# Performance work log

Hardware: AMD Instinct MI355X
Metric: run time of the kernel (lower is better)

## Reference

```python
import jax, jax.numpy as jnp
import numpy as np

B, T, H = 4096, 64, 64        # sequences, time_step, n_hidden
OBS, ACT = 128, 32
EPS = 1e-12                    # tf.contrib layer_norm epsilon


def layer_norm(x, g, b):
    m = x.mean(-1, keepdims=True)
    v = x.var(-1, keepdims=True)
    return (x - m) * jax.lax.rsqrt(v + EPS) * g + b


def lstm_scan(xs, W, b):
    # xs: [T, B, D_in]; BasicLSTMCell with forget_bias=1.0
    h0 = jnp.zeros((xs.shape[1], H), xs.dtype)
    c0 = h0
    def step(carry, x_t):
        h, c = carry
        z = jnp.concatenate([x_t, h], axis=-1) @ W + b   # [B, 4H]
        i, j, f, o = jnp.split(z, 4, axis=-1)
        c = c * jax.nn.sigmoid(f + 1.0) + jax.nn.sigmoid(i) * jnp.tanh(j)
        h = jnp.tanh(c) * jax.nn.sigmoid(o)
        return (h, c), h
    _, hs = jax.lax.scan(step, (h0, c0), xs)
    return hs  # [T, B, H]


def setup_inputs() -> dict:
    key = jax.random.key(0)
    ks = jax.random.split(key, 10)
    u = lambda k, shp, s: jax.random.uniform(k, shp, jnp.float32, -s, s)
    return dict(
        obs=jax.random.normal(ks[0], (B * T, OBS), jnp.float32),
        action=jax.random.normal(ks[1], (B * T, ACT), jnp.float32),
        W1=u(ks[2], (OBS, 64), 0.1), b1=jnp.zeros(64), g1=jnp.ones(64), be1=jnp.zeros(64),
        W2=u(ks[3], (64 + ACT, 64), 0.1), b2=jnp.zeros(64), g2=jnp.ones(64), be2=jnp.zeros(64),
        Wf=u(ks[4], (64 + H, 4 * H), 0.08), bf=jnp.zeros(4 * H),
        Wb=u(ks[5], (64 + H, 4 * H), 0.08), bb=jnp.zeros(4 * H),
        wx=u(ks[6], (H,), 0.003), bx=jnp.zeros(()),
        wp=u(ks[7], (H,), 0.003), bp=jnp.zeros(()),
        gp=jnp.ones(T), bep=jnp.zeros(T),
        W3=u(ks[8], (T, T), 0.003), b3=jnp.zeros(T),
    )


def reference(obs, action, W1, b1, g1, be1, W2, b2, g2, be2,
              Wf, bf, Wb, bb, wx, bx, wp, bp, gp, bep, W3, b3):
    # MLP trunk
    x = jax.nn.relu(layer_norm(obs @ W1 + b1, g1, be1))
    x = jnp.concatenate([x, action], axis=-1)
    x = jax.nn.relu(layer_norm(x @ W2 + b2, g2, be2))
    # [B*T, 64] -> [T, B, 64] for scan
    x = x.reshape(B, T, 64).transpose(1, 0, 2)
    h_fw = lstm_scan(x, Wf, bf)                 # [T, B, H]
    h_bw = lstm_scan(x[::-1], Wb, bb)[::-1]     # [T, B, H]
    # tf.reshape of the (fw, bw) tuple stacks -> [2, B, T, H] -> [2B, T*H, 1]
    h = jnp.concatenate([h_fw.transpose(1, 0, 2), h_bw.transpose(1, 0, 2)], axis=0)  # [2B, T, H]
    # conv1d(kernel=H, stride=H) over flattened T*H axis == per-timestep dot
    xs = jnp.einsum('btd,d->bt', h, wx) + bx    # [2B, T] values
    ps = jnp.einsum('btd,d->bt', h, wp) + bp    # [2B, T] attention logits
    p = jax.nn.relu(layer_norm(ps, gp, bep))
    p = jax.nn.softmax(p @ W3 + b3, axis=-1)
    return jnp.sum(p * xs, axis=1)              # [2B]
```

## Files before the change

kernel.cpp:

```cpp
#include <hip/hip_runtime.h>
#include <hip/hip_bf16.h>

typedef __attribute__((ext_vector_type(8))) short s16x8;
typedef __attribute__((ext_vector_type(4))) float f32x4;
typedef __attribute__((ext_vector_type(4))) unsigned int u32x4;

#define MFMA(a,b,c) __builtin_amdgcn_mfma_f32_16x16x32_bf16((a),(b),(c),0,0,0)

__device__ __forceinline__ unsigned short bf16_rne(float f){
  unsigned int u = __float_as_uint(f);
  return (unsigned short)((u + 0x7FFFu + ((u >> 16) & 1u)) >> 16);
}
__device__ __forceinline__ float bf16_f32(unsigned short h){
  return __uint_as_float(((unsigned int)h) << 16);
}
__device__ __forceinline__ void split_hl(float f, short& hi, short& lo){
  unsigned short h = bf16_rne(f);
  float rem = f - bf16_f32(h);
  hi = (short)h;
  lo = (short)bf16_rne(rem);
}

__device__ __forceinline__ unsigned int cvt_pk_bf16(float a, float b){
  unsigned int r;
  asm("v_cvt_pk_bf16_f32 %0, %1, %2" : "=v"(r) : "v"(a), "v"(b));
  return r;
}

__device__ __forceinline__ void build_frag(const float* p, s16x8& fh, s16x8& fl){
  float4 v0 = *(const float4*)p;
  float4 v1 = *(const float4*)(p + 4);
  float vv[8] = {v0.x, v0.y, v0.z, v0.w, v1.x, v1.y, v1.z, v1.w};
  u32x4 th, tl;
  #pragma unroll
  for(int q = 0; q < 4; ++q){
    unsigned int h2 = cvt_pk_bf16(vv[2*q], vv[2*q+1]);
    float r0 = vv[2*q]     - __uint_as_float(h2 << 16);
    float r1 = vv[2*q + 1] - __uint_as_float(h2 & 0xffff0000u);
    th[q] = h2;
    tl[q] = cvt_pk_bf16(r0, r1);
  }
  fh = __builtin_bit_cast(s16x8, th);
  fl = __builtin_bit_cast(s16x8, tl);
}

__device__ __forceinline__ float sigm(float x){
  return __builtin_amdgcn_rcpf(1.0f + __expf(-x));
}
__device__ __forceinline__ float tanh_fast(float x){
  return 1.0f - 2.0f * __builtin_amdgcn_rcpf(__expf(2.0f * x) + 1.0f);
}

__global__ __launch_bounds__(256) void pack_kernel(
    const float* __restrict__ W1, const float* __restrict__ W2,
    const float* __restrict__ Wf, const float* __restrict__ Wb,
    unsigned short* __restrict__ w1p, unsigned short* __restrict__ w2p,
    unsigned short* __restrict__ wfp, unsigned short* __restrict__ wbp)
{
  int id = blockIdx.x * 256 + threadIdx.x;
  if(id < 8192){
    int t = id;
    int j = t & 7, lane = (t >> 3) & 63, nt = (t >> 9) & 3, kk = t >> 11;
    int k = kk * 32 + 8 * (lane >> 4) + j;
    int col = nt * 16 + (lane & 15);
    short h, l; split_hl(W1[k * 64 + col], h, l);
    w1p[t] = (unsigned short)h; w1p[8192 + t] = (unsigned short)l;
  } else if(id < 14336){
    int t = id - 8192;
    int j = t & 7, lane = (t >> 3) & 63, nt = (t >> 9) & 3, kk = t >> 11;
    int k = kk * 32 + 8 * (lane >> 4) + j;
    int col = nt * 16 + (lane & 15);
    short h, l; split_hl(W2[k * 64 + col], h, l);
    w2p[t] = (unsigned short)h; w2p[6144 + t] = (unsigned short)l;
  } else if(id < 47104){
    int t = id - 14336;
    int j = t & 7, lane = (t >> 3) & 63, dj = (t >> 9) & 3, kk = (t >> 11) & 3, gi = t >> 13;
    int k = kk * 32 + 8 * (lane >> 4) + j;
    int col = gi * 64 + dj * 16 + (lane & 15);
    short h, l; split_hl(Wf[k * 256 + col], h, l);
    wfp[t] = (unsigned short)h; wfp[32768 + t] = (unsigned short)l;
  } else if(id < 79872){
    int t = id - 47104;
    int j = t & 7, lane = (t >> 3) & 63, dj = (t >> 9) & 3, kk = (t >> 11) & 3, gi = t >> 13;
    int k = kk * 32 + 8 * (lane >> 4) + j;
    int col = gi * 64 + dj * 16 + (lane & 15);
    short h, l; split_hl(Wb[k * 256 + col], h, l);
    wbp[t] = (unsigned short)h; wbp[32768 + t] = (unsigned short)l;
  }
}

__global__ __launch_bounds__(256) void trunk_kernel(
    const float* __restrict__ obs, const float* __restrict__ actg,
    const float* __restrict__ b1, const float* __restrict__ g1, const float* __restrict__ be1,
    const float* __restrict__ b2, const float* __restrict__ g2, const float* __restrict__ be2,
    const unsigned short* __restrict__ w1p, const unsigned short* __restrict__ w2p,
    unsigned short* __restrict__ x2h, unsigned short* __restrict__ x2l)
{
  __shared__ __align__(16) float x1_t[64][68];

  const int tid = threadIdx.x;
  const int r0 = blockIdx.x * 64;
  const int w = tid >> 6, lane = tid & 63;
  const int l15 = lane & 15, l4 = lane >> 4;

  float b1v[4], g1v[4], be1v[4], b2v[4], g2v[4], be2v[4];
  #pragma unroll
  for(int nt = 0; nt < 4; ++nt){
    int col = nt * 16 + l15;
    b1v[nt] = b1[col]; g1v[nt] = g1[col]; be1v[nt] = be1[col];
    b2v[nt] = b2[col]; g2v[nt] = g2[col]; be2v[nt] = be2[col];
  }

  f32x4 acc1[4] = {{0,0,0,0},{0,0,0,0},{0,0,0,0},{0,0,0,0}};
  #pragma unroll
  for(int kk = 0; kk < 4; ++kk){
    s16x8 ah, al;
    build_frag(&obs[(size_t)(r0 + w * 16 + l15) * 128 + 8 * l4 + 32 * kk], ah, al);
    #pragma unroll
    for(int nt = 0; nt < 4; ++nt){
      s16x8 bh = *(const s16x8*)&w1p[(kk * 2048 + nt * 512) + lane * 8];
      s16x8 bl = *(const s16x8*)&w1p[8192 + (kk * 2048 + nt * 512) + lane * 8];
      acc1[nt] = MFMA(ah, bh, acc1[nt]);
      acc1[nt] = MFMA(ah, bl, acc1[nt]);
      acc1[nt] = MFMA(al, bh, acc1[nt]);
    }
  }

  #pragma unroll
  for(int r = 0; r < 4; ++r){
    float v[4];
    #pragma unroll
    for(int nt = 0; nt < 4; ++nt) v[nt] = acc1[nt][r] + b1v[nt];
    float s = (v[0] + v[1]) + (v[2] + v[3]);
    #pragma unroll
    for(int mm = 1; mm < 16; mm <<= 1) s += __shfl_xor(s, mm);
    float mean = s * (1.0f / 64.0f);
    float d[4]; float q = 0.f;
    #pragma unroll
    for(int nt = 0; nt < 4; ++nt){ d[nt] = v[nt] - mean; q += d[nt] * d[nt]; }
    #pragma unroll
    for(int mm = 1; mm < 16; mm <<= 1) q += __shfl_xor(q, mm);
    float rstd = rsqrtf(q * (1.0f / 64.0f) + 1e-12f);
    int row = w * 16 + l4 * 4 + r;
    #pragma unroll
    for(int nt = 0; nt < 4; ++nt)
      x1_t[row][nt * 16 + l15] = fmaxf(0.f, d[nt] * rstd * g1v[nt] + be1v[nt]);
  }
  __syncthreads();

  f32x4 acc2[4] = {{0,0,0,0},{0,0,0,0},{0,0,0,0},{0,0,0,0}};
  #pragma unroll
  for(int kk = 0; kk < 3; ++kk){
    s16x8 ah, al;
    if(kk < 2) build_frag(&x1_t[w * 16 + l15][8 * l4 + 32 * kk], ah, al);
    else       build_frag(&actg[(size_t)(r0 + w * 16 + l15) * 32 + 8 * l4], ah, al);
    #pragma unroll
    for(int nt = 0; nt < 4; ++nt){
      s16x8 bh = *(const s16x8*)&w2p[(kk * 2048 + nt * 512) + lane * 8];
      s16x8 bl = *(const s16x8*)&w2p[6144 + (kk * 2048 + nt * 512) + lane * 8];
      acc2[nt] = MFMA(ah, bh, acc2[nt]);
      acc2[nt] = MFMA(ah, bl, acc2[nt]);
      acc2[nt] = MFMA(al, bh, acc2[nt]);
    }
  }

  #pragma unroll
  for(int r = 0; r < 4; ++r){
    float v[4];
    #pragma unroll
    for(int nt = 0; nt < 4; ++nt) v[nt] = acc2[nt][r] + b2v[nt];
    float s = (v[0] + v[1]) + (v[2] + v[3]);
    #pragma unroll
    for(int mm = 1; mm < 16; mm <<= 1) s += __shfl_xor(s, mm);
    float mean = s * (1.0f / 64.0f);
    float d[4]; float q = 0.f;
    #pragma unroll
    for(int nt = 0; nt < 4; ++nt){ d[nt] = v[nt] - mean; q += d[nt] * d[nt]; }
    #pragma unroll
    for(int mm = 1; mm < 16; mm <<= 1) q += __shfl_xor(q, mm);
    float rstd = rsqrtf(q * (1.0f / 64.0f) + 1e-12f);
    size_t rowg = (size_t)(r0 + w * 16 + l4 * 4 + r);
    float xv[4];
    #pragma unroll
    for(int nt = 0; nt < 4; ++nt) xv[nt] = fmaxf(0.f, d[nt] * rstd * g2v[nt] + be2v[nt]);
    unsigned int ph01 = cvt_pk_bf16(xv[0], xv[1]);
    float q0 = xv[0] - __uint_as_float(ph01 << 16);
    float q1 = xv[1] - __uint_as_float(ph01 & 0xffff0000u);
    unsigned int pl01 = cvt_pk_bf16(q0, q1);
    unsigned int ph23 = cvt_pk_bf16(xv[2], xv[3]);
    float q2 = xv[2] - __uint_as_float(ph23 << 16);
    float q3 = xv[3] - __uint_as_float(ph23 & 0xffff0000u);
    unsigned int pl23 = cvt_pk_bf16(q2, q3);
    x2h[rowg * 64 +  0 + l15] = (unsigned short)ph01;
    x2h[rowg * 64 + 16 + l15] = (unsigned short)(ph01 >> 16);
    x2h[rowg * 64 + 32 + l15] = (unsigned short)ph23;
    x2h[rowg * 64 + 48 + l15] = (unsigned short)(ph23 >> 16);
    x2l[rowg * 64 +  0 + l15] = (unsigned short)pl01;
    x2l[rowg * 64 + 16 + l15] = (unsigned short)(pl01 >> 16);
    x2l[rowg * 64 + 32 + l15] = (unsigned short)pl23;
    x2l[rowg * 64 + 48 + l15] = (unsigned short)(pl23 >> 16);
  }
}

__global__ __launch_bounds__(256, 2) void lstm_kernel(
    const unsigned short* __restrict__ x2h, const unsigned short* __restrict__ x2l,
    const unsigned short* __restrict__ wfp, const unsigned short* __restrict__ wbp,
    const float* __restrict__ bfv, const float* __restrict__ bbv,
    const float* __restrict__ wx, const float* __restrict__ wp,
    const float* __restrict__ bx, const float* __restrict__ bp,
    const float* __restrict__ gp, const float* __restrict__ bep,
    const float* __restrict__ W3, const float* __restrict__ b3,
    float* __restrict__ out)
{
  __shared__ __align__(16) unsigned short h_h[2][16][72];
  __shared__ __align__(16) unsigned short h_l[2][16][72];
  __shared__ float xs_sh[16][64];
  __shared__ float ps_sh[16][64];
  __shared__ float W3s[64][64];
  __shared__ float p_sh[4][64];

  const int tid = threadIdx.x;
  const int dir = blockIdx.y;
  const int b0 = blockIdx.x * 16;
  const unsigned short* wpk  = dir ? wbp : wfp;
  const float* bias = dir ? bbv : bfv;

  const int w = tid >> 6, lane = tid & 63, l15 = lane & 15, l4 = lane >> 4;
  const int dj = w;

  float biasv[4];
  #pragma unroll
  for(int gi = 0; gi < 4; ++gi) biasv[gi] = bias[gi * 64 + dj * 16 + l15];
  biasv[2] += 1.0f;

  s16x8 Bh[4][4], Bl[4][4];
  #pragma unroll
  for(int gi = 0; gi < 4; ++gi){
    #pragma unroll
    for(int kk = 0; kk < 4; ++kk){
      int off = ((gi * 4 + kk) * 4 + dj) * 512 + lane * 8;
      Bh[gi][kk] = *(const s16x8*)&wpk[off];
      Bl[gi][kk] = *(const s16x8*)&wpk[32768 + off];
      asm volatile("" : "+v"(Bh[gi][kk]), "+v"(Bl[gi][kk]));
    }
  }

  s16x8 Bx[2];
  #pragma unroll
  for(int kk = 0; kk < 2; ++kk){
    #pragma unroll
    for(int j = 0; j < 8; ++j){
      int k = kk * 32 + 8 * l4 + j;
      short xh, xl, ph, pl;
      split_hl(wx[k], xh, xl);
      split_hl(wp[k], ph, pl);
      short sel = (l15 == 0) ? xh : (l15 == 1) ? xl : (l15 == 2) ? ph : (l15 == 3) ? pl : (short)0;
      Bx[kk][j] = sel;
    }
  }

  #pragma unroll
  for(int i = 0; i < 4; ++i)
    *(float4*)&W3s[0][tid * 16 + i * 4] = *(const float4*)&W3[tid * 16 + i * 4];
  for(int i = tid; i < 16 * 72; i += 256){
    (&h_h[0][0][0])[i] = 0; (&h_l[0][0][0])[i] = 0;
  }

  const unsigned short* xbh = x2h + (size_t)(b0 + l15) * 4096 + 8 * l4;
  const unsigned short* xbl = x2l + (size_t)(b0 + l15) * 4096 + 8 * l4;

  int t0 = dir ? 63 : 0;
  int t1 = dir ? 62 : 1;
  s16x8 xah  = *(const s16x8*)&xbh[t0 * 64];
  s16x8 xah2 = *(const s16x8*)&xbh[t0 * 64 + 32];
  s16x8 xal  = *(const s16x8*)&xbl[t0 * 64];
  s16x8 xal2 = *(const s16x8*)&xbl[t0 * 64 + 32];
  s16x8 xbhr = *(const s16x8*)&xbh[t1 * 64];
  s16x8 xbh2 = *(const s16x8*)&xbh[t1 * 64 + 32];
  s16x8 xblr = *(const s16x8*)&xbl[t1 * 64];
  s16x8 xbl2 = *(const s16x8*)&xbl[t1 * 64 + 32];

  float c[4] = {0.f, 0.f, 0.f, 0.f};

  __syncthreads();

  auto lstm_step = [&](s16x8& XH0, s16x8& XH1, s16x8& XL0, s16x8& XL1, int tau){
    const int cb = tau & 1, nb = cb ^ 1;
    s16x8 Ahh0 = *(const s16x8*)&h_h[cb][l15][8 * l4];
    s16x8 Ahh1 = *(const s16x8*)&h_h[cb][l15][8 * l4 + 32];
    s16x8 Ahl0 = *(const s16x8*)&h_l[cb][l15][8 * l4];
    s16x8 Ahl1 = *(const s16x8*)&h_l[cb][l15][8 * l4 + 32];
    f32x4 acc[4];
    #pragma unroll
    for(int gi = 0; gi < 4; ++gi)
      acc[gi] = (f32x4){biasv[gi], biasv[gi], biasv[gi], biasv[gi]};
    __builtin_amdgcn_s_setprio(1);
    #pragma unroll
    for(int gi = 0; gi < 4; ++gi){
      acc[gi] = MFMA(XH0, Bh[gi][0], acc[gi]);
      acc[gi] = MFMA(XH0, Bl[gi][0], acc[gi]);
      acc[gi] = MFMA(XL0, Bh[gi][0], acc[gi]);
      acc[gi] = MFMA(XH1, Bh[gi][1], acc[gi]);
      acc[gi] = MFMA(XH1, Bl[gi][1], acc[gi]);
      acc[gi] = MFMA(XL1, Bh[gi][1], acc[gi]);
    }
    __builtin_amdgcn_s_setprio(0);
    {
      int tf = tau + 2; if(tf > 63) tf = 63;
      int tn = dir ? 63 - tf : tf;
      XH0 = *(const s16x8*)&xbh[tn * 64];
      XH1 = *(const s16x8*)&xbh[tn * 64 + 32];
      XL0 = *(const s16x8*)&xbl[tn * 64];
      XL1 = *(const s16x8*)&xbl[tn * 64 + 32];
    }
    f32x4 accd = {0.f, 0.f, 0.f, 0.f};
    __builtin_amdgcn_s_setprio(1);
    #pragma unroll
    for(int gi = 0; gi < 4; ++gi){
      acc[gi] = MFMA(Ahh0, Bh[gi][2], acc[gi]);
      acc[gi] = MFMA(Ahh0, Bl[gi][2], acc[gi]);
      acc[gi] = MFMA(Ahl0, Bh[gi][2], acc[gi]);
      acc[gi] = MFMA(Ahh1, Bh[gi][3], acc[gi]);
      acc[gi] = MFMA(Ahh1, Bl[gi][3], acc[gi]);
      acc[gi] = MFMA(Ahl1, Bh[gi][3], acc[gi]);
    }
    if(dj == 0){
      accd = MFMA(Ahh0, Bx[0], accd);
      accd = MFMA(Ahl0, Bx[0], accd);
      accd = MFMA(Ahh1, Bx[1], accd);
      accd = MFMA(Ahl1, Bx[1], accd);
    }
    __builtin_amdgcn_s_setprio(0);
    if(dj == 0 && tau > 0){
      int tp = dir ? 64 - tau : tau - 1;
      #pragma unroll
      for(int r = 0; r < 4; ++r){
        float v = accd[r] + __shfl_xor(accd[r], 1);
        int s = l4 * 4 + r;
        if(l15 == 0) xs_sh[s][tp] = v;
        else if(l15 == 2) ps_sh[s][tp] = v;
      }
    }
    float hv[4];
    #pragma unroll
    for(int r = 0; r < 4; ++r){
      float zi = acc[0][r];
      float zj = acc[1][r];
      float zf = acc[2][r];
      float zo = acc[3][r];
      float cf = c[r] * sigm(zf) + sigm(zi) * tanh_fast(zj);
      c[r] = cf;
      hv[r] = tanh_fast(cf) * sigm(zo);
    }
    {
      unsigned int ph01 = cvt_pk_bf16(hv[0], hv[1]);
      float q0 = hv[0] - __uint_as_float(ph01 << 16);
      float q1 = hv[1] - __uint_as_float(ph01 & 0xffff0000u);
      unsigned int pl01 = cvt_pk_bf16(q0, q1);
      unsigned int ph23 = cvt_pk_bf16(hv[2], hv[3]);
      float q2 = hv[2] - __uint_as_float(ph23 << 16);
      float q3 = hv[3] - __uint_as_float(ph23 & 0xffff0000u);
      unsigned int pl23 = cvt_pk_bf16(q2, q3);
      int sb = l4 * 4, col = dj * 16 + l15;
      h_h[nb][sb + 0][col] = (unsigned short)ph01;
      h_h[nb][sb + 1][col] = (unsigned short)(ph01 >> 16);
      h_h[nb][sb + 2][col] = (unsigned short)ph23;
      h_h[nb][sb + 3][col] = (unsigned short)(ph23 >> 16);
      h_l[nb][sb + 0][col] = (unsigned short)pl01;
      h_l[nb][sb + 1][col] = (unsigned short)(pl01 >> 16);
      h_l[nb][sb + 2][col] = (unsigned short)pl23;
      h_l[nb][sb + 3][col] = (unsigned short)(pl23 >> 16);
    }
    __syncthreads();
  };

  for(int tau = 0; tau < 64; tau += 2){
    lstm_step(xah, xah2, xal, xal2, tau);
    lstm_step(xbhr, xbh2, xblr, xbl2, tau + 1);
  }

  if(dj == 0){
    s16x8 Ahh0 = *(const s16x8*)&h_h[0][l15][8 * l4];
    s16x8 Ahh1 = *(const s16x8*)&h_h[0][l15][8 * l4 + 32];
    s16x8 Ahl0 = *(const s16x8*)&h_l[0][l15][8 * l4];
    s16x8 Ahl1 = *(const s16x8*)&h_l[0][l15][8 * l4 + 32];
    f32x4 accd = {0.f, 0.f, 0.f, 0.f};
    accd = MFMA(Ahh0, Bx[0], accd);
    accd = MFMA(Ahl0, Bx[0], accd);
    accd = MFMA(Ahh1, Bx[1], accd);
    accd = MFMA(Ahl1, Bx[1], accd);
    int tp = dir ? 0 : 63;
    #pragma unroll
    for(int r = 0; r < 4; ++r){
      float v = accd[r] + __shfl_xor(accd[r], 1);
      int s = l4 * 4 + r;
      if(l15 == 0) xs_sh[s][tp] = v;
      else if(l15 == 2) ps_sh[s][tp] = v;
    }
  }
  __syncthreads();

  const float bxv = bx[0], bpv = bp[0];
  #pragma unroll
  for(int r = 0; r < 4; ++r){
    int s = w * 4 + r;
    float xsv = xs_sh[s][lane] + bxv;
    float psv = ps_sh[s][lane] + bpv;
    float sum = psv;
    #pragma unroll
    for(int mm = 1; mm < 64; mm <<= 1) sum += __shfl_xor(sum, mm);
    float mean = sum * (1.f / 64.f);
    float d = psv - mean;
    float q = d * d;
    #pragma unroll
    for(int mm = 1; mm < 64; mm <<= 1) q += __shfl_xor(q, mm);
    float rstd = rsqrtf(q * (1.f / 64.f) + 1e-12f);
    float p = fmaxf(0.f, d * rstd * gp[lane] + bep[lane]);
    p_sh[w][lane] = p;
    float logit = b3[lane];
    #pragma unroll 8
    for(int t = 0; t < 64; ++t) logit += p_sh[w][t] * W3s[t][lane];
    float mx = logit;
    #pragma unroll
    for(int mm = 1; mm < 64; mm <<= 1) mx = fmaxf(mx, __shfl_xor(mx, mm));
    float e = __expf(logit - mx);
    float se = e;
    #pragma unroll
    for(int mm = 1; mm < 64; mm <<= 1) se += __shfl_xor(se, mm);
    float contrib = (e / se) * xsv;
    #pragma unroll
    for(int mm = 1; mm < 64; mm <<= 1) contrib += __shfl_xor(contrib, mm);
    if(lane == 0) out[(size_t)dir * 4096 + b0 + s] = contrib;
  }
}

extern "C" void kernel_launch(void* const* d_in, const int* in_sizes, int n_in,
                              void* d_out, int out_size, void* d_ws, size_t ws_size,
                              hipStream_t stream)
{
  (void)in_sizes; (void)n_in; (void)out_size; (void)ws_size;
  const float* obs = (const float*)d_in[0];
  const float* act = (const float*)d_in[1];
  const float* W1  = (const float*)d_in[2];
  const float* b1  = (const float*)d_in[3];
  const float* g1  = (const float*)d_in[4];
  const float* be1 = (const float*)d_in[5];
  const float* W2  = (const float*)d_in[6];
  const float* b2  = (const float*)d_in[7];
  const float* g2  = (const float*)d_in[8];
  const float* be2 = (const float*)d_in[9];
  const float* Wf  = (const float*)d_in[10];
  const float* bfv = (const float*)d_in[11];
  const float* Wb  = (const float*)d_in[12];
  const float* bbv = (const float*)d_in[13];
  const float* wx  = (const float*)d_in[14];
  const float* bx  = (const float*)d_in[15];
  const float* wp  = (const float*)d_in[16];
  const float* bp  = (const float*)d_in[17];
  const float* gp  = (const float*)d_in[18];
  const float* bep = (const float*)d_in[19];
  const float* W3  = (const float*)d_in[20];
  const float* b3  = (const float*)d_in[21];

  unsigned short* x2h = (unsigned short*)d_ws;
  unsigned short* x2l = x2h + (size_t)262144 * 64;
  unsigned short* w1p = x2l + (size_t)262144 * 64;
  unsigned short* w2p = w1p + 2 * 8192;
  unsigned short* wfp = w2p + 2 * 6144;
  unsigned short* wbp = wfp + 2 * 32768;
  float* outf = (float*)d_out;

  pack_kernel<<<312, 256, 0, stream>>>(W1, W2, Wf, Wb, w1p, w2p, wfp, wbp);
  trunk_kernel<<<4096, 256, 0, stream>>>(obs, act, b1, g1, be1, b2, g2, be2, w1p, w2p, x2h, x2l);
  lstm_kernel<<<dim3(256, 2), 256, 0, stream>>>(x2h, x2l, wfp, wbp, bfv, bbv, wx, wp,
                                                bx, bp, gp, bep, W3, b3, outf);
}
```

Baseline: 183.0 us.

## Split LSTM block into input-projection and recurrent warp groups via LDS

Doubles the LSTM block to 512 threads. Four warps compute the input projection x_t·W_x one step ahead and pass it through a double-buffered LDS array. The other four warps run only the recurrent h·W_h MFMAs plus the gate math. This takes the input-projection MFMAs off the serial recurrence critical path and halves the weight registers per thread. In exchange it adds LDS traffic and a larger block that may lower occupancy per CU.

```diff
diff --git a/kernel.cpp b/kernel.cpp
--- a/kernel.cpp
+++ b/kernel.cpp
@@ -202,7 +202,7 @@
   }
 }
 
-__global__ __launch_bounds__(256, 2) void lstm_kernel(
+__global__ __launch_bounds__(512, 4) void lstm_kernel(
     const unsigned short* __restrict__ x2h, const unsigned short* __restrict__ x2l,
     const unsigned short* __restrict__ wfp, const unsigned short* __restrict__ wbp,
     const float* __restrict__ bfv, const float* __restrict__ bbv,
@@ -214,10 +214,11 @@
 {
   __shared__ __align__(16) unsigned short h_h[2][16][72];
   __shared__ __align__(16) unsigned short h_l[2][16][72];
+  __shared__ __align__(16) float zxs[2][4][4][64][4];
   __shared__ float xs_sh[16][64];
   __shared__ float ps_sh[16][64];
   __shared__ float W3s[64][64];
-  __shared__ float p_sh[4][64];
+  __shared__ float p_sh[8][64];
 
   const int tid = threadIdx.x;
   const int dir = blockIdx.y;
@@ -226,169 +227,195 @@
   const float* bias = dir ? bbv : bfv;
 
   const int w = tid >> 6, lane = tid & 63, l15 = lane & 15, l4 = lane >> 4;
-  const int dj = w;
+  const int dj = w & 3, kh = w >> 2;
+
+  s16x8 Bh[4][2], Bl[4][2];
+  #pragma unroll
+  for(int gi = 0; gi < 4; ++gi){
+    #pragma unroll
+    for(int kki = 0; kki < 2; ++kki){
+      int kk = kh * 2 + kki;
+      int off = ((gi * 4 + kk) * 4 + dj) * 512 + lane * 8;
+      Bh[gi][kki] = *(const s16x8*)&wpk[off];
+      Bl[gi][kki] = *(const s16x8*)&wpk[32768 + off];
+      asm volatile("" : "+v"(Bh[gi][kki]), "+v"(Bl[gi][kki]));
+    }
+  }
 
   float biasv[4];
   #pragma unroll
   for(int gi = 0; gi < 4; ++gi) biasv[gi] = bias[gi * 64 + dj * 16 + l15];
   biasv[2] += 1.0f;
 
-  s16x8 Bh[4][4], Bl[4][4];
-  #pragma unroll
-  for(int gi = 0; gi < 4; ++gi){
-    #pragma unroll
-    for(int kk = 0; kk < 4; ++kk){
-      int off = ((gi * 4 + kk) * 4 + dj) * 512 + lane * 8;
-      Bh[gi][kk] = *(const s16x8*)&wpk[off];
-      Bl[gi][kk] = *(const s16x8*)&wpk[32768 + off];
-      asm volatile("" : "+v"(Bh[gi][kk]), "+v"(Bl[gi][kk]));
-    }
-  }
-
-  s16x8 Bx[2];
-  #pragma unroll
-  for(int kk = 0; kk < 2; ++kk){
-    #pragma unroll
-    for(int j = 0; j < 8; ++j){
-      int k = kk * 32 + 8 * l4 + j;
-      short xh, xl, ph, pl;
-      split_hl(wx[k], xh, xl);
-      split_hl(wp[k], ph, pl);
-      short sel = (l15 == 0) ? xh : (l15 == 1) ? xl : (l15 == 2) ? ph : (l15 == 3) ? pl : (short)0;
-      Bx[kk][j] = sel;
-    }
-  }
-
-  #pragma unroll
-  for(int i = 0; i < 4; ++i)
-    *(float4*)&W3s[0][tid * 16 + i * 4] = *(const float4*)&W3[tid * 16 + i * 4];
-  for(int i = tid; i < 16 * 72; i += 256){
+  s16x8 Bx0, Bx1;
+  if(kh == 1 && dj == 0){
+    #pragma unroll
+    for(int kki = 0; kki < 2; ++kki){
+      s16x8 t;
+      #pragma unroll
+      for(int j = 0; j < 8; ++j){
+        int k = kki * 32 + 8 * l4 + j;
+        short xh, xl, ph, pl;
+        split_hl(wx[k], xh, xl);
+        split_hl(wp[k], ph, pl);
+        t[j] = (l15 == 0) ? xh : (l15 == 1) ? xl : (l15 == 2) ? ph : (l15 == 3) ? pl : (short)0;
+      }
+      if(kki == 0) Bx0 = t; else Bx1 = t;
+    }
+  }
+
+  *(float4*)&W3s[0][tid * 8]     = *(const float4*)&W3[tid * 8];
+  *(float4*)&W3s[0][tid * 8 + 4] = *(const float4*)&W3[tid * 8 + 4];
+  for(int i = tid; i < 16 * 72; i += 512){
     (&h_h[0][0][0])[i] = 0; (&h_l[0][0][0])[i] = 0;
   }
 
   const unsigned short* xbh = x2h + (size_t)(b0 + l15) * 4096 + 8 * l4;
   const unsigned short* xbl = x2l + (size_t)(b0 + l15) * 4096 + 8 * l4;
 
-  int t0 = dir ? 63 : 0;
-  int t1 = dir ? 62 : 1;
-  s16x8 xah  = *(const s16x8*)&xbh[t0 * 64];
-  s16x8 xah2 = *(const s16x8*)&xbh[t0 * 64 + 32];
-  s16x8 xal  = *(const s16x8*)&xbl[t0 * 64];
-  s16x8 xal2 = *(const s16x8*)&xbl[t0 * 64 + 32];
-  s16x8 xbhr = *(const s16x8*)&xbh[t1 * 64];
-  s16x8 xbh2 = *(const s16x8*)&xbh[t1 * 64 + 32];
-  s16x8 xblr = *(const s16x8*)&xbl[t1 * 64];
-  s16x8 xbl2 = *(const s16x8*)&xbl[t1 * 64 + 32];
-
-  float c[4] = {0.f, 0.f, 0.f, 0.f};
-
-  __syncthreads();
-
-  auto lstm_step = [&](s16x8& XH0, s16x8& XH1, s16x8& XL0, s16x8& XL1, int tau){
-    const int cb = tau & 1, nb = cb ^ 1;
-    s16x8 Ahh0 = *(const s16x8*)&h_h[cb][l15][8 * l4];
-    s16x8 Ahh1 = *(const s16x8*)&h_h[cb][l15][8 * l4 + 32];
-    s16x8 Ahl0 = *(const s16x8*)&h_l[cb][l15][8 * l4];
-    s16x8 Ahl1 = *(const s16x8*)&h_l[cb][l15][8 * l4 + 32];
+  s16x8 xh0, xh1, xl0, xl1;
+  if(kh == 0){
+    int tn0 = dir ? 63 : 0;
+    xh0 = *(const s16x8*)&xbh[tn0 * 64];
+    xh1 = *(const s16x8*)&xbh[tn0 * 64 + 32];
+    xl0 = *(const s16x8*)&xbl[tn0 * 64];
+    xl1 = *(const s16x8*)&xbl[tn0 * 64 + 32];
     f32x4 acc[4];
     #pragma unroll
     for(int gi = 0; gi < 4; ++gi)
       acc[gi] = (f32x4){biasv[gi], biasv[gi], biasv[gi], biasv[gi]};
-    __builtin_amdgcn_s_setprio(1);
     #pragma unroll
     for(int gi = 0; gi < 4; ++gi){
-      acc[gi] = MFMA(XH0, Bh[gi][0], acc[gi]);
-      acc[gi] = MFMA(XH0, Bl[gi][0], acc[gi]);
-      acc[gi] = MFMA(XL0, Bh[gi][0], acc[gi]);
-      acc[gi] = MFMA(XH1, Bh[gi][1], acc[gi]);
-      acc[gi] = MFMA(XH1, Bl[gi][1], acc[gi]);
-      acc[gi] = MFMA(XL1, Bh[gi][1], acc[gi]);
-    }
-    __builtin_amdgcn_s_setprio(0);
-    {
-      int tf = tau + 2; if(tf > 63) tf = 63;
-      int tn = dir ? 63 - tf : tf;
-      XH0 = *(const s16x8*)&xbh[tn * 64];
-      XH1 = *(const s16x8*)&xbh[tn * 64 + 32];
-      XL0 = *(const s16x8*)&xbl[tn * 64];
-      XL1 = *(const s16x8*)&xbl[tn * 64 + 32];
-    }
-    f32x4 accd = {0.f, 0.f, 0.f, 0.f};
-    __builtin_amdgcn_s_setprio(1);
-    #pragma unroll
-    for(int gi = 0; gi < 4; ++gi){
-      acc[gi] = MFMA(Ahh0, Bh[gi][2], acc[gi]);
-      acc[gi] = MFMA(Ahh0, Bl[gi][2], acc[gi]);
-      acc[gi] = MFMA(Ahl0, Bh[gi][2], acc[gi]);
-      acc[gi] = MFMA(Ahh1, Bh[gi][3], acc[gi]);
-      acc[gi] = MFMA(Ahh1, Bl[gi][3], acc[gi]);
-      acc[gi] = MFMA(Ahl1, Bh[gi][3], acc[gi]);
-    }
-    if(dj == 0){
-      accd = MFMA(Ahh0, Bx[0], accd);
-      accd = MFMA(Ahl0, Bx[0], accd);
-      accd = MFMA(Ahh1, Bx[1], accd);
-      accd = MFMA(Ahl1, Bx[1], accd);
-    }
-    __builtin_amdgcn_s_setprio(0);
-    if(dj == 0 && tau > 0){
-      int tp = dir ? 64 - tau : tau - 1;
+      acc[gi] = MFMA(xh0, Bh[gi][0], acc[gi]);
+      acc[gi] = MFMA(xh0, Bl[gi][0], acc[gi]);
+      acc[gi] = MFMA(xl0, Bh[gi][0], acc[gi]);
+      acc[gi] = MFMA(xh1, Bh[gi][1], acc[gi]);
+      acc[gi] = MFMA(xh1, Bl[gi][1], acc[gi]);
+      acc[gi] = MFMA(xl1, Bh[gi][1], acc[gi]);
+    }
+    #pragma unroll
+    for(int gi = 0; gi < 4; ++gi)
+      *(f32x4*)&zxs[0][gi][dj][lane][0] = acc[gi];
+    int tn1 = dir ? 62 : 1;
+    xh0 = *(const s16x8*)&xbh[tn1 * 64];
+    xh1 = *(const s16x8*)&xbh[tn1 * 64 + 32];
+    xl0 = *(const s16x8*)&xbl[tn1 * 64];
+    xl1 = *(const s16x8*)&xbl[tn1 * 64 + 32];
+  }
+
+  float c[4] = {0.f, 0.f, 0.f, 0.f};
+  __syncthreads();
+
+  for(int tau = 0; tau < 64; ++tau){
+    const int cb = tau & 1, nb = cb ^ 1;
+    if(kh == 0){
+      if(tau < 63){
+        f32x4 acc[4];
+        #pragma unroll
+        for(int gi = 0; gi < 4; ++gi)
+          acc[gi] = (f32x4){biasv[gi], biasv[gi], biasv[gi], biasv[gi]};
+        __builtin_amdgcn_s_setprio(1);
+        #pragma unroll
+        for(int gi = 0; gi < 4; ++gi){
+          acc[gi] = MFMA(xh0, Bh[gi][0], acc[gi]);
+          acc[gi] = MFMA(xh0, Bl[gi][0], acc[gi]);
+          acc[gi] = MFMA(xl0, Bh[gi][0], acc[gi]);
+          acc[gi] = MFMA(xh1, Bh[gi][1], acc[gi]);
+          acc[gi] = MFMA(xh1, Bl[gi][1], acc[gi]);
+          acc[gi] = MFMA(xl1, Bh[gi][1], acc[gi]);
+        }
+        __builtin_amdgcn_s_setprio(0);
+        int tf = tau + 2; if(tf > 63) tf = 63;
+        int tn = dir ? 63 - tf : tf;
+        xh0 = *(const s16x8*)&xbh[tn * 64];
+        xh1 = *(const s16x8*)&xbh[tn * 64 + 32];
+        xl0 = *(const s16x8*)&xbl[tn * 64];
+        xl1 = *(const s16x8*)&xbl[tn * 64 + 32];
+        #pragma unroll
+        for(int gi = 0; gi < 4; ++gi)
+          *(f32x4*)&zxs[nb][gi][dj][lane][0] = acc[gi];
+      }
+    } else {
+      s16x8 Ahh0 = *(const s16x8*)&h_h[cb][l15][8 * l4];
+      s16x8 Ahh1 = *(const s16x8*)&h_h[cb][l15][8 * l4 + 32];
+      s16x8 Ahl0 = *(const s16x8*)&h_l[cb][l15][8 * l4];
+      s16x8 Ahl1 = *(const s16x8*)&h_l[cb][l15][8 * l4 + 32];
+      f32x4 acc[4];
+      #pragma unroll
+      for(int gi = 0; gi < 4; ++gi)
+        acc[gi] = *(const f32x4*)&zxs[cb][gi][dj][lane][0];
+      f32x4 accd = {0.f, 0.f, 0.f, 0.f};
+      __builtin_amdgcn_s_setprio(1);
+      #pragma unroll
+      for(int gi = 0; gi < 4; ++gi){
+        acc[gi] = MFMA(Ahh0, Bh[gi][0], acc[gi]);
+        acc[gi] = MFMA(Ahh0, Bl[gi][0], acc[gi]);
+        acc[gi] = MFMA(Ahl0, Bh[gi][0], acc[gi]);
+        acc[gi] = MFMA(Ahh1, Bh[gi][1], acc[gi]);
+        acc[gi] = MFMA(Ahh1, Bl[gi][1], acc[gi]);
+        acc[gi] = MFMA(Ahl1, Bh[gi][1], acc[gi]);
+      }
+      if(dj == 0){
+        accd = MFMA(Ahh0, Bx0, accd);
+        accd = MFMA(Ahl0, Bx0, accd);
+        accd = MFMA(Ahh1, Bx1, accd);
+        accd = MFMA(Ahl1, Bx1, accd);
+      }
+      __builtin_amdgcn_s_setprio(0);
+      if(dj == 0 && tau > 0){
+        int tp = dir ? 64 - tau : tau - 1;
+        #pragma unroll
+        for(int r = 0; r < 4; ++r){
+          float v = accd[r] + __shfl_xor(accd[r], 1);
+          int s = l4 * 4 + r;
+          if(l15 == 0) xs_sh[s][tp] = v;
+          else if(l15 == 2) ps_sh[s][tp] = v;
+        }
+      }
+      float hv[4];
       #pragma unroll
       for(int r = 0; r < 4; ++r){
-        float v = accd[r] + __shfl_xor(accd[r], 1);
-        int s = l4 * 4 + r;
-        if(l15 == 0) xs_sh[s][tp] = v;
-        else if(l15 == 2) ps_sh[s][tp] = v;
-      }
-    }
-    float hv[4];
-    #pragma unroll
-    for(int r = 0; r < 4; ++r){
-      float zi = acc[0][r];
-      float zj = acc[1][r];
-      float zf = acc[2][r];
-      float zo = acc[3][r];
-      float cf = c[r] * sigm(zf) + sigm(zi) * tanh_fast(zj);
-      c[r] = cf;
-      hv[r] = tanh_fast(cf) * sigm(zo);
-    }
-    {
-      unsigned int ph01 = cvt_pk_bf16(hv[0], hv[1]);
-      float q0 = hv[0] - __uint_as_float(ph01 << 16);
-      float q1 = hv[1] - __uint_as_float(ph01 & 0xffff0000u);
-      unsigned int pl01 = cvt_pk_bf16(q0, q1);
-      unsigned int ph23 = cvt_pk_bf16(hv[2], hv[3]);
-      float q2 = hv[2] - __uint_as_float(ph23 << 16);
-      float q3 = hv[3] - __uint_as_float(ph23 & 0xffff0000u);
-      unsigned int pl23 = cvt_pk_bf16(q2, q3);
-      int sb = l4 * 4, col = dj * 16 + l15;
-      h_h[nb][sb + 0][col] = (unsigned short)ph01;
-      h_h[nb][sb + 1][col] = (unsigned short)(ph01 >> 16);
-      h_h[nb][sb + 2][col] = (unsigned short)ph23;
-      h_h[nb][sb + 3][col] = (unsigned short)(ph23 >> 16);
-      h_l[nb][sb + 0][col] = (unsigned short)pl01;
-      h_l[nb][sb + 1][col] = (unsigned short)(pl01 >> 16);
-      h_l[nb][sb + 2][col] = (unsigned short)pl23;
-      h_l[nb][sb + 3][col] = (unsigned short)(pl23 >> 16);
+        float zi = acc[0][r];
+        float zj = acc[1][r];
+        float zf = acc[2][r];
+        float zo = acc[3][r];
+        float cf = c[r] * sigm(zf) + sigm(zi) * tanh_fast(zj);
+        c[r] = cf;
+        hv[r] = tanh_fast(cf) * sigm(zo);
+      }
+      {
+        unsigned int ph01 = cvt_pk_bf16(hv[0], hv[1]);
+        float q0 = hv[0] - __uint_as_float(ph01 << 16);
+        float q1 = hv[1] - __uint_as_float(ph01 & 0xffff0000u);
+        unsigned int pl01 = cvt_pk_bf16(q0, q1);
+        unsigned int ph23 = cvt_pk_bf16(hv[2], hv[3]);
+        float q2 = hv[2] - __uint_as_float(ph23 << 16);
+        float q3 = hv[3] - __uint_as_float(ph23 & 0xffff0000u);
+        unsigned int pl23 = cvt_pk_bf16(q2, q3);
+        int sb = l4 * 4, col = dj * 16 + l15;
+        h_h[nb][sb + 0][col] = (unsigned short)ph01;
+        h_h[nb][sb + 1][col] = (unsigned short)(ph01 >> 16);
+        h_h[nb][sb + 2][col] = (unsigned short)ph23;
+        h_h[nb][sb + 3][col] = (unsigned short)(ph23 >> 16);
+        h_l[nb][sb + 0][col] = (unsigned short)pl01;
+        h_l[nb][sb + 1][col] = (unsigned short)(pl01 >> 16);
+        h_l[nb][sb + 2][col] = (unsigned short)pl23;
+        h_l[nb][sb + 3][col] = (unsigned short)(pl23 >> 16);
+      }
     }
     __syncthreads();
-  };
-
-  for(int tau = 0; tau < 64; tau += 2){
-    lstm_step(xah, xah2, xal, xal2, tau);
-    lstm_step(xbhr, xbh2, xblr, xbl2, tau + 1);
-  }
-
-  if(dj == 0){
+  }
+
+  if(kh == 1 && dj == 0){
     s16x8 Ahh0 = *(const s16x8*)&h_h[0][l15][8 * l4];
     s16x8 Ahh1 = *(const s16x8*)&h_h[0][l15][8 * l4 + 32];
     s16x8 Ahl0 = *(const s16x8*)&h_l[0][l15][8 * l4];
     s16x8 Ahl1 = *(const s16x8*)&h_l[0][l15][8 * l4 + 32];
     f32x4 accd = {0.f, 0.f, 0.f, 0.f};
-    accd = MFMA(Ahh0, Bx[0], accd);
-    accd = MFMA(Ahl0, Bx[0], accd);
-    accd = MFMA(Ahh1, Bx[1], accd);
-    accd = MFMA(Ahl1, Bx[1], accd);
+    accd = MFMA(Ahh0, Bx0, accd);
+    accd = MFMA(Ahl0, Bx0, accd);
+    accd = MFMA(Ahh1, Bx1, accd);
+    accd = MFMA(Ahl1, Bx1, accd);
     int tp = dir ? 0 : 63;
     #pragma unroll
     for(int r = 0; r < 4; ++r){
@@ -402,8 +429,8 @@
 
   const float bxv = bx[0], bpv = bp[0];
   #pragma unroll
-  for(int r = 0; r < 4; ++r){
-    int s = w * 4 + r;
+  for(int r = 0; r < 2; ++r){
+    int s = w * 2 + r;
     float xsv = xs_sh[s][lane] + bxv;
     float psv = ps_sh[s][lane] + bpv;
     float sum = psv;
@@ -472,6 +499,6 @@
 
   pack_kernel<<<312, 256, 0, stream>>>(W1, W2, Wf, Wb, w1p, w2p, wfp, wbp);
   trunk_kernel<<<4096, 256, 0, stream>>>(obs, act, b1, g1, be1, b2, g2, be2, w1p, w2p, x2h, x2l);
-  lstm_kernel<<<dim3(256, 2), 256, 0, stream>>>(x2h, x2l, wfp, wbp, bfv, bbv, wx, wp,
+  lstm_kernel<<<dim3(256, 2), 512, 0, stream>>>(x2h, x2l, wfp, wbp, bfv, bbv, wx, wp,
                                                 bx, bp, gp, bep, W3, b3, outf);
 }
```

After: 427.3 us. +133.5%, slower.

## Precompute next-step input projection after h write and stream input weights

Applied to the files above, without the earlier changes.

Each LSTM step now starts from an input projection zx that was already computed, so after the barrier only the recurrent h·W MFMAs and the gate math remain. The input projection for the next timestep is computed after h is written to shared memory and before the barrier. The input-half weights are no longer held in registers; they are reloaded from global memory every step, which lowers register pressure but adds per-step cache traffic. The per-step MFMA count is unchanged and the barrier still waits for the extra work, so the gain depends on latency hiding and occupancy.

```diff
diff --git a/kernel.cpp b/kernel.cpp
--- a/kernel.cpp
+++ b/kernel.cpp
@@ -233,29 +233,32 @@
   for(int gi = 0; gi < 4; ++gi) biasv[gi] = bias[gi * 64 + dj * 16 + l15];
   biasv[2] += 1.0f;
 
-  s16x8 Bh[4][4], Bl[4][4];
+  s16x8 WhH[4][2], WhL[4][2];
   #pragma unroll
   for(int gi = 0; gi < 4; ++gi){
     #pragma unroll
-    for(int kk = 0; kk < 4; ++kk){
-      int off = ((gi * 4 + kk) * 4 + dj) * 512 + lane * 8;
-      Bh[gi][kk] = *(const s16x8*)&wpk[off];
-      Bl[gi][kk] = *(const s16x8*)&wpk[32768 + off];
-      asm volatile("" : "+v"(Bh[gi][kk]), "+v"(Bl[gi][kk]));
-    }
-  }
-
-  s16x8 Bx[2];
-  #pragma unroll
-  for(int kk = 0; kk < 2; ++kk){
-    #pragma unroll
-    for(int j = 0; j < 8; ++j){
-      int k = kk * 32 + 8 * l4 + j;
-      short xh, xl, ph, pl;
-      split_hl(wx[k], xh, xl);
-      split_hl(wp[k], ph, pl);
-      short sel = (l15 == 0) ? xh : (l15 == 1) ? xl : (l15 == 2) ? ph : (l15 == 3) ? pl : (short)0;
-      Bx[kk][j] = sel;
+    for(int kki = 0; kki < 2; ++kki){
+      int off = ((gi * 4 + 2 + kki) * 4 + dj) * 512 + lane * 8;
+      WhH[gi][kki] = *(const s16x8*)&wpk[off];
+      WhL[gi][kki] = *(const s16x8*)&wpk[32768 + off];
+      asm volatile("" : "+v"(WhH[gi][kki]), "+v"(WhL[gi][kki]));
+    }
+  }
+
+  s16x8 Bx0, Bx1;
+  if(dj == 0){
+    #pragma unroll
+    for(int kki = 0; kki < 2; ++kki){
+      s16x8 t;
+      #pragma unroll
+      for(int j = 0; j < 8; ++j){
+        int k = kki * 32 + 8 * l4 + j;
+        short xh, xl, ph, pl;
+        split_hl(wx[k], xh, xl);
+        split_hl(wp[k], ph, pl);
+        t[j] = (l15 == 0) ? xh : (l15 == 1) ? xl : (l15 == 2) ? ph : (l15 == 3) ? pl : (short)0;
+      }
+      if(kki == 0) Bx0 = t; else Bx1 = t;
     }
   }
 
@@ -269,22 +272,40 @@
   const unsigned short* xbh = x2h + (size_t)(b0 + l15) * 4096 + 8 * l4;
   const unsigned short* xbl = x2l + (size_t)(b0 + l15) * 4096 + 8 * l4;
 
-  int t0 = dir ? 63 : 0;
-  int t1 = dir ? 62 : 1;
-  s16x8 xah  = *(const s16x8*)&xbh[t0 * 64];
-  s16x8 xah2 = *(const s16x8*)&xbh[t0 * 64 + 32];
-  s16x8 xal  = *(const s16x8*)&xbl[t0 * 64];
-  s16x8 xal2 = *(const s16x8*)&xbl[t0 * 64 + 32];
-  s16x8 xbhr = *(const s16x8*)&xbh[t1 * 64];
-  s16x8 xbh2 = *(const s16x8*)&xbh[t1 * 64 + 32];
-  s16x8 xblr = *(const s16x8*)&xbl[t1 * 64];
-  s16x8 xbl2 = *(const s16x8*)&xbl[t1 * 64 + 32];
+  int t0i = dir ? 63 : 0;
+  s16x8 xh0 = *(const s16x8*)&xbh[t0i * 64];
+  s16x8 xh1 = *(const s16x8*)&xbh[t0i * 64 + 32];
+  s16x8 xl0 = *(const s16x8*)&xbl[t0i * 64];
+  s16x8 xl1 = *(const s16x8*)&xbl[t0i * 64 + 32];
+  f32x4 zx[4];
+  #pragma unroll
+  for(int gi = 0; gi < 4; ++gi){
+    zx[gi] = (f32x4){biasv[gi], biasv[gi], biasv[gi], biasv[gi]};
+    int off0 = ((gi * 4 + 0) * 4 + dj) * 512 + lane * 8;
+    int off1 = ((gi * 4 + 1) * 4 + dj) * 512 + lane * 8;
+    s16x8 b0h = *(const s16x8*)&wpk[off0];
+    s16x8 b0l = *(const s16x8*)&wpk[32768 + off0];
+    s16x8 b1h = *(const s16x8*)&wpk[off1];
+    s16x8 b1l = *(const s16x8*)&wpk[32768 + off1];
+    zx[gi] = MFMA(xh0, b0h, zx[gi]);
+    zx[gi] = MFMA(xh0, b0l, zx[gi]);
+    zx[gi] = MFMA(xl0, b0h, zx[gi]);
+    zx[gi] = MFMA(xh1, b1h, zx[gi]);
+    zx[gi] = MFMA(xh1, b1l, zx[gi]);
+    zx[gi] = MFMA(xl1, b1h, zx[gi]);
+  }
+  {
+    int t1i = dir ? 62 : 1;
+    xh0 = *(const s16x8*)&xbh[t1i * 64];
+    xh1 = *(const s16x8*)&xbh[t1i * 64 + 32];
+    xl0 = *(const s16x8*)&xbl[t1i * 64];
+    xl1 = *(const s16x8*)&xbl[t1i * 64 + 32];
+  }
 
   float c[4] = {0.f, 0.f, 0.f, 0.f};
-
   __syncthreads();
 
-  auto lstm_step = [&](s16x8& XH0, s16x8& XH1, s16x8& XL0, s16x8& XL1, int tau){
+  for(int tau = 0; tau < 64; ++tau){
     const int cb = tau & 1, nb = cb ^ 1;
     s16x8 Ahh0 = *(const s16x8*)&h_h[cb][l15][8 * l4];
     s16x8 Ahh1 = *(const s16x8*)&h_h[cb][l15][8 * l4 + 32];
@@ -292,54 +313,14 @@
     s16x8 Ahl1 = *(const s16x8*)&h_l[cb][l15][8 * l4 + 32];
     f32x4 acc[4];
     #pragma unroll
-    for(int gi = 0; gi < 4; ++gi)
-      acc[gi] = (f32x4){biasv[gi], biasv[gi], biasv[gi], biasv[gi]};
-    __builtin_amdgcn_s_setprio(1);
-    #pragma unroll
     for(int gi = 0; gi < 4; ++gi){
-      acc[gi] = MFMA(XH0, Bh[gi][0], acc[gi]);
-      acc[gi] = MFMA(XH0, Bl[gi][0], acc[gi]);
-      acc[gi] = MFMA(XL0, Bh[gi][0], acc[gi]);
-      acc[gi] = MFMA(XH1, Bh[gi][1], acc[gi]);
-      acc[gi] = MFMA(XH1, Bl[gi][1], acc[gi]);
-      acc[gi] = MFMA(XL1, Bh[gi][1], acc[gi]);
-    }
-    __builtin_amdgcn_s_setprio(0);
-    {
-      int tf = tau + 2; if(tf > 63) tf = 63;
-      int tn = dir ? 63 - tf : tf;
-      XH0 = *(const s16x8*)&xbh[tn * 64];
-      XH1 = *(const s16x8*)&xbh[tn * 64 + 32];
-      XL0 = *(const s16x8*)&xbl[tn * 64];
-      XL1 = *(const s16x8*)&xbl[tn * 64 + 32];
-    }
-    f32x4 accd = {0.f, 0.f, 0.f, 0.f};
-    __builtin_amdgcn_s_setprio(1);
-    #pragma unroll
-    for(int gi = 0; gi < 4; ++gi){
-      acc[gi] = MFMA(Ahh0, Bh[gi][2], acc[gi]);
-      acc[gi] = MFMA(Ahh0, Bl[gi][2], acc[gi]);
-      acc[gi] = MFMA(Ahl0, Bh[gi][2], acc[gi]);
-      acc[gi] = MFMA(Ahh1, Bh[gi][3], acc[gi]);
-      acc[gi] = MFMA(Ahh1, Bl[gi][3], acc[gi]);
-      acc[gi] = MFMA(Ahl1, Bh[gi][3], acc[gi]);
-    }
-    if(dj == 0){
-      accd = MFMA(Ahh0, Bx[0], accd);
-      accd = MFMA(Ahl0, Bx[0], accd);
-      accd = MFMA(Ahh1, Bx[1], accd);
-      accd = MFMA(Ahl1, Bx[1], accd);
-    }
-    __builtin_amdgcn_s_setprio(0);
-    if(dj == 0 && tau > 0){
-      int tp = dir ? 64 - tau : tau - 1;
-      #pragma unroll
-      for(int r = 0; r < 4; ++r){
-        float v = accd[r] + __shfl_xor(accd[r], 1);
-        int s = l4 * 4 + r;
-        if(l15 == 0) xs_sh[s][tp] = v;
-        else if(l15 == 2) ps_sh[s][tp] = v;
-      }
+      acc[gi] = zx[gi];
+      acc[gi] = MFMA(Ahh0, WhH[gi][0], acc[gi]);
+      acc[gi] = MFMA(Ahh0, WhL[gi][0], acc[gi]);
+      acc[gi] = MFMA(Ahl0, WhH[gi][0], acc[gi]);
+      acc[gi] = MFMA(Ahh1, WhH[gi][1], acc[gi]);
+      acc[gi] = MFMA(Ahh1, WhL[gi][1], acc[gi]);
+      acc[gi] = MFMA(Ahl1, WhH[gi][1], acc[gi]);
     }
     float hv[4];
     #pragma unroll
@@ -371,12 +352,48 @@
       h_l[nb][sb + 2][col] = (unsigned short)pl23;
       h_l[nb][sb + 3][col] = (unsigned short)(pl23 >> 16);
     }
+    if(dj == 0){
+      f32x4 accd = {0.f, 0.f, 0.f, 0.f};
+      accd = MFMA(Ahh0, Bx0, accd);
+      accd = MFMA(Ahl0, Bx0, accd);
+      accd = MFMA(Ahh1, Bx1, accd);
+      accd = MFMA(Ahl1, Bx1, accd);
+      if(tau > 0){
+        int tp = dir ? 64 - tau : tau - 1;
+        #pragma unroll
+        for(int r = 0; r < 4; ++r){
+          float v = accd[r] + __shfl_xor(accd[r], 1);
+          int s = l4 * 4 + r;
+          if(l15 == 0) xs_sh[s][tp] = v;
+          else if(l15 == 2) ps_sh[s][tp] = v;
+        }
+      }
+    }
+    if(tau < 63){
+      #pragma unroll
+      for(int gi = 0; gi < 4; ++gi){
+        zx[gi] = (f32x4){biasv[gi], biasv[gi], biasv[gi], biasv[gi]};
+        int off0 = ((gi * 4 + 0) * 4 + dj) * 512 + lane * 8;
+        int off1 = ((gi * 4 + 1) * 4 + dj) * 512 + lane * 8;
+        s16x8 b0h = *(const s16x8*)&wpk[off0];
+        s16x8 b0l = *(const s16x8*)&wpk[32768 + off0];
+        s16x8 b1h = *(const s16x8*)&wpk[off1];
+        s16x8 b1l = *(const s16x8*)&wpk[32768 + off1];
+        zx[gi] = MFMA(xh0, b0h, zx[gi]);
+        zx[gi] = MFMA(xh0, b0l, zx[gi]);
+        zx[gi] = MFMA(xl0, b0h, zx[gi]);
+        zx[gi] = MFMA(xh1, b1h, zx[gi]);
+        zx[gi] = MFMA(xh1, b1l, zx[gi]);
+        zx[gi] = MFMA(xl1, b1h, zx[gi]);
+      }
+      int tf = tau + 2; if(tf > 63) tf = 63;
+      int tn = dir ? 63 - tf : tf;
+      xh0 = *(const s16x8*)&xbh[tn * 64];
+      xh1 = *(const s16x8*)&xbh[tn * 64 + 32];
+      xl0 = *(const s16x8*)&xbl[tn * 64];
+      xl1 = *(const s16x8*)&xbl[tn * 64 + 32];
+    }
     __syncthreads();
-  };
-
-  for(int tau = 0; tau < 64; tau += 2){
-    lstm_step(xah, xah2, xal, xal2, tau);
-    lstm_step(xbhr, xbh2, xblr, xbl2, tau + 1);
   }
 
   if(dj == 0){
@@ -385,10 +402,10 @@
     s16x8 Ahl0 = *(const s16x8*)&h_l[0][l15][8 * l4];
     s16x8 Ahl1 = *(const s16x8*)&h_l[0][l15][8 * l4 + 32];
     f32x4 accd = {0.f, 0.f, 0.f, 0.f};
-    accd = MFMA(Ahh0, Bx[0], accd);
-    accd = MFMA(Ahl0, Bx[0], accd);
-    accd = MFMA(Ahh1, Bx[1], accd);
-    accd = MFMA(Ahl1, Bx[1], accd);
+    accd = MFMA(Ahh0, Bx0, accd);
+    accd = MFMA(Ahl0, Bx0, accd);
+    accd = MFMA(Ahh1, Bx1, accd);
+    accd = MFMA(Ahl1, Bx1, accd);
     int tp = dir ? 0 : 63;
     #pragma unroll
     for(int r = 0; r < 4; ++r){
```

Result: slower. 221.2 us (+20.9%).
